# Kernel optimization log

Measured on AMD Instinct MI355X. Metric: run time of the kernel, lower is better.

The kernel has to match this reference:

```python
import jax, jax.numpy as jnp
import numpy as np
from jax import lax

DN = ('NCHW', 'OIHW', 'NCHW')
EPS = 1e-5  # PyTorch BatchNorm default eps


def _bn(x, g, b):
    # BatchNorm2d in training mode: batch statistics over (N, H, W), biased var
    m = jnp.mean(x, (0, 2, 3), keepdims=True)
    v = jnp.mean((x - m) ** 2, (0, 2, 3), keepdims=True)
    return (x - m) * lax.rsqrt(v + EPS) * g[None, :, None, None] + b[None, :, None, None]


def _conv(x, w, b):
    # Conv2d(k=4, stride=2, padding=1)
    y = lax.conv_general_dilated(x, w, (2, 2), ((1, 1), (1, 1)), dimension_numbers=DN)
    return y + b[None, :, None, None]


def _deconv(x, w, b):
    # ConvTranspose2d(k=4, stride=2, padding=1) == dilated-input conv, pad k-1-p=2
    y = lax.conv_general_dilated(x, w, (1, 1), ((2, 2), (2, 2)), lhs_dilation=(2, 2),
                                 dimension_numbers=DN)
    return y + b[None, :, None, None]


def reference(x, codebook, eW1, eb1, eg1, ebt1, eW2, eb2, eg2, ebt2, eW3, eb3, eg3, ebt3,
              dW1, db1, dg1, dbt1, dW2, db2, dg2, dbt2, dW3, db3, dg3, dbt3):
    # --- encoder ---
    h = jax.nn.relu(_bn(_conv(x, eW1, eb1), eg1, ebt1))
    h = jax.nn.relu(_bn(_conv(h, eW2, eb2), eg2, ebt2))
    z_e = jax.nn.relu(_bn(_conv(h, eW3, eb3), eg3, ebt3))  # [B, 64, H/8, W/8]
    # --- vector quantization ---
    zp = z_e.transpose(0, 2, 3, 1)                 # [B, h, w, D]
    D = zp.shape[-1]
    z = zp.reshape(-1, D)                          # [N, D]
    dist = (jnp.sum(z * z, axis=1, keepdims=True)
            + jnp.sum(codebook * codebook, axis=1)
            - 2.0 * (z @ codebook.T))              # [N, K] squared distances
    idx = jnp.argmin(dist, axis=1)                 # [N]
    quant = codebook[idx].reshape(zp.shape)        # gather == one-hot matmul
    e_loss = jnp.mean((lax.stop_gradient(quant) - zp) ** 2)
    q_loss = jnp.mean((quant - lax.stop_gradient(zp)) ** 2)
    loss = q_loss + e_loss
    # straight-through estimator
    q_st = (zp + lax.stop_gradient(quant - zp)).transpose(0, 3, 1, 2)  # [B, D, h, w]
    # --- decoder ---
    h = jax.nn.relu(_bn(_deconv(q_st, dW1, db1), dg1, dbt1))
    h = jax.nn.relu(_bn(_deconv(h, dW2, db2), dg2, dbt2))
    z_d = jnp.tanh(_bn(_deconv(h, dW3, db3), dg3, dbt3))
    return z_d, loss


def setup_inputs() -> dict:
    key = jax.random.key(0)
    ks = jax.random.split(key, 16)
    B, C, H, W = 64, 3, 256, 256
    K, D = 512, 64
    f32 = jnp.float32

    def w(k, shape, fan_in):
        return jax.random.normal(k, shape, f32) * np.float32(1.0 / np.sqrt(fan_in))

    inp = {}
    inp['x'] = jax.random.normal(ks[0], (B, C, H, W), f32)
    inp['codebook'] = jax.random.uniform(ks[1], (K, D), f32, -1.0 / K, 1.0 / K)
    # encoder: 3 -> 16 -> 32 -> 64, conv k=4
    inp['eW1'] = w(ks[2], (16, 3, 4, 4), 3 * 16);   inp['eb1'] = jnp.zeros(16, f32)
    inp['eg1'] = jnp.ones(16, f32);                 inp['ebt1'] = jnp.zeros(16, f32)
    inp['eW2'] = w(ks[3], (32, 16, 4, 4), 16 * 16); inp['eb2'] = jnp.zeros(32, f32)
    inp['eg2'] = jnp.ones(32, f32);                 inp['ebt2'] = jnp.zeros(32, f32)
    inp['eW3'] = w(ks[4], (64, 32, 4, 4), 32 * 16); inp['eb3'] = jnp.zeros(64, f32)
    inp['eg3'] = jnp.ones(64, f32);                 inp['ebt3'] = jnp.zeros(64, f32)
    # decoder: 64 -> 32 -> 16 -> 3, convtranspose k=4 (weights stored OIHW)
    inp['dW1'] = w(ks[5], (32, 64, 4, 4), 64 * 16); inp['db1'] = jnp.zeros(32, f32)
    inp['dg1'] = jnp.ones(32, f32);                 inp['dbt1'] = jnp.zeros(32, f32)
    inp['dW2'] = w(ks[6], (16, 32, 4, 4), 32 * 16); inp['db2'] = jnp.zeros(16, f32)
    inp['dg2'] = jnp.ones(16, f32);                 inp['dbt2'] = jnp.zeros(16, f32)
    inp['dW3'] = w(ks[7], (3, 16, 4, 4), 16 * 16);  inp['db3'] = jnp.zeros(3, f32)
    inp['dg3'] = jnp.ones(3, f32);                  inp['dbt3'] = jnp.zeros(3, f32)
    return inp
```

## Files before the change

### kernel.cpp

```cpp
#include <hip/hip_runtime.h>
#include <hip/hip_bf16.h>


#define EPS 1e-5

__global__ void zero_stats_k(double* s, int n) {
    int i = blockIdx.x * blockDim.x + threadIdx.x;
    if (i < n) s[i] = 0.0;
}

__global__ void convert_w_k(const float* __restrict__ w1, const float* __restrict__ w2,
                            const float* __restrict__ w3, double* __restrict__ w64) {
    int i = blockIdx.x * blockDim.x + threadIdx.x;
    if (i < 768) w64[i] = (double)w1[i];
    else if (i < 768 + 8192) w64[i] = (double)w2[i - 768];
    else if (i < 768 + 8192 + 32768) w64[i] = (double)w3[i - 768 - 8192];
}

__device__ __forceinline__ void block_reduce2(double v1, double v2,
                                              double* t1, double* t2) {
#pragma unroll
    for (int o = 32; o; o >>= 1) {
        v1 += __shfl_down(v1, o);
        v2 += __shfl_down(v2, o);
    }
    __shared__ double ls[4][2];
    int wid = threadIdx.x >> 6, lane = threadIdx.x & 63;
    if (lane == 0) { ls[wid][0] = v1; ls[wid][1] = v2; }
    __syncthreads();
    if (threadIdx.x == 0) {
        atomicAdd(t1, ls[0][0] + ls[1][0] + ls[2][0] + ls[3][0]);
        atomicAdd(t2, ls[0][1] + ls[1][1] + ls[2][1] + ls[3][1]);
    }
    __syncthreads();
}

__global__ void conv1_stats_k(const float* __restrict__ x, const double* __restrict__ w64,
                              const float* __restrict__ bias,
                              double* __restrict__ partials) {
    __shared__ float xs[3][6][258];
    __shared__ double lsw[4][32];
    int band = blockIdx.x, n = blockIdx.y, tid = threadIdx.x;
    double sums[16], sqs[16];
#pragma unroll
    for (int j = 0; j < 16; ++j) { sums[j] = 0.0; sqs[j] = 0.0; }
    for (int s8 = 0; s8 < 8; ++s8) {
        int strip = band * 8 + s8;
        int iyBase = 4 * strip - 1;
        __syncthreads();
        for (int idx = tid; idx < 3 * 6 * 258; idx += 256) {
            int ch = idx / 1548, rem = idx - ch * 1548, r = rem / 258, cc = rem - r * 258;
            int iy = iyBase + r, ix = cc - 1;
            float v = 0.f;
            if ((unsigned)iy < 256u && (unsigned)ix < 256u)
                v = x[(size_t)(n * 3 + ch) * 65536 + iy * 256 + ix];
            xs[ch][r][cc] = v;
        }
        __syncthreads();
        int lr = 2 * (tid >> 7), lc = 2 * (tid & 127);
        double xd[3][4][4];
#pragma unroll
        for (int ci = 0; ci < 3; ++ci)
#pragma unroll
            for (int ky = 0; ky < 4; ++ky)
#pragma unroll
                for (int kx = 0; kx < 4; ++kx)
                    xd[ci][ky][kx] = (double)xs[ci][lr + ky][lc + kx];
#pragma unroll
        for (int co = 0; co < 16; ++co) {
            double acc = (double)bias[co];
            const double* wp = w64 + co * 48;
#pragma unroll
            for (int ci = 0; ci < 3; ++ci)
#pragma unroll
                for (int ky = 0; ky < 4; ++ky)
#pragma unroll
                    for (int kx = 0; kx < 4; ++kx)
                        acc = fma(xd[ci][ky][kx], wp[ci * 16 + ky * 4 + kx], acc);
            sums[co] += acc;
            sqs[co] = fma(acc, acc, sqs[co]);
        }
    }
    double val[32];
#pragma unroll
    for (int j = 0; j < 16; ++j) { val[j] = sums[j]; val[16 + j] = sqs[j]; }
#pragma unroll
    for (int o = 32; o; o >>= 1)
#pragma unroll
        for (int j = 0; j < 32; ++j) val[j] += __shfl_down(val[j], o);
    int wid = tid >> 6, lane = tid & 63;
    if (lane == 0)
#pragma unroll
        for (int j = 0; j < 32; ++j) lsw[wid][j] = val[j];
    __syncthreads();
    if (tid < 32) {
        double p = lsw[0][tid] + lsw[1][tid] + lsw[2][tid] + lsw[3][tid];
        partials[(size_t)(n * 8 + band) * 32 + tid] = p;
    }
}

__global__ void reduce_stats_k(const double* __restrict__ partials,
                               double* __restrict__ stats) {
    int t = threadIdx.x;
    if (t < 32) {
        double s = 0.0;
        for (int i = 0; i < 512; ++i) s += partials[(size_t)i * 32 + t];
        stats[t] = s;
    }
}

__global__ void fused_conv2_k(const float* __restrict__ x, const double* __restrict__ w1_64,
                              const float* __restrict__ eb1, const float* __restrict__ eg1,
                              const float* __restrict__ ebt1, const double* __restrict__ w2_64,
                              const float* __restrict__ eb2, const double* __restrict__ stats,
                              float* __restrict__ h2) {
    __shared__ float xs[3][38][38];
    __shared__ float h1s[16][18][18];
    int tile = blockIdx.x, n = blockIdx.y, tid = threadIdx.x;
    int ty = tile >> 3, tx = tile & 7;
    int iyBase = 32 * ty - 3, ixBase = 32 * tx - 3;
    for (int idx = tid; idx < 3 * 38 * 38; idx += 256) {
        int ch = idx / 1444, rem = idx - ch * 1444, r = rem / 38, cc = rem - r * 38;
        int iy = iyBase + r, ix = ixBase + cc;
        float v = 0.f;
        if ((unsigned)iy < 256u && (unsigned)ix < 256u)
            v = x[(size_t)(n * 3 + ch) * 65536 + iy * 256 + ix];
        xs[ch][r][cc] = v;
    }
    __syncthreads();
    int hy0 = 16 * ty - 1, hx0 = 16 * tx - 1;
    for (int idx = tid; idx < 16 * 18 * 18; idx += 256) {
        int ci = idx / 324, rem = idx - ci * 324, r = rem / 18, cc = rem - r * 18;
        int hy = hy0 + r, hx = hx0 + cc;
        float val = 0.f;
        if ((unsigned)hy < 128u && (unsigned)hx < 128u) {
            double xd[3][4][4];
#pragma unroll
            for (int c3 = 0; c3 < 3; ++c3)
#pragma unroll
                for (int ky = 0; ky < 4; ++ky)
#pragma unroll
                    for (int kx = 0; kx < 4; ++kx)
                        xd[c3][ky][kx] = (double)xs[c3][2 * r + ky][2 * cc + kx];
            double acc = (double)eb1[ci];
            const double* wp = w1_64 + ci * 48;
#pragma unroll
            for (int c3 = 0; c3 < 3; ++c3)
#pragma unroll
                for (int ky = 0; ky < 4; ++ky)
#pragma unroll
                    for (int kx = 0; kx < 4; ++kx)
                        acc = fma(xd[c3][ky][kx], wp[c3 * 16 + ky * 4 + kx], acc);
            double m = stats[ci] * (1.0 / 1048576.0);
            double var = stats[16 + ci] * (1.0 / 1048576.0) - m * m;
            double sc = (double)eg1[ci] / sqrt(var + EPS);
            double sh = (double)ebt1[ci] - m * sc;
            double v = fma(acc, sc, sh);
            val = (float)(v > 0.0 ? v : 0.0);
        }
        h1s[ci][r][cc] = val;
    }
    __syncthreads();
    int s = tid & 63, ly = s >> 3, lx = s & 7;
    int cog = __builtin_amdgcn_readfirstlane((tid >> 6) * 8);
    double acc[8];
#pragma unroll
    for (int j = 0; j < 8; ++j) acc[j] = (double)eb2[cog + j];
    for (int ci = 0; ci < 16; ++ci) {
        double td[16];
#pragma unroll
        for (int ky = 0; ky < 4; ++ky)
#pragma unroll
            for (int kx = 0; kx < 4; ++kx)
                td[ky * 4 + kx] = (double)h1s[ci][2 * ly + ky][2 * lx + kx];
#pragma unroll
        for (int j = 0; j < 8; ++j) {
            const double* wp = w2_64 + ((cog + j) * 16 + ci) * 16;
#pragma unroll
            for (int k = 0; k < 16; ++k)
                acc[j] = fma(td[k], wp[k], acc[j]);
        }
    }
    int oy = 8 * ty + ly, ox = 8 * tx + lx;
#pragma unroll
    for (int j = 0; j < 8; ++j)
        h2[(size_t)(n * 32 + cog + j) * 4096 + oy * 64 + ox] = (float)acc[j];
}

__global__ void bn_stats_k(const float* __restrict__ y, double* __restrict__ sum,
                           double* __restrict__ sq, int C, int HW) {
    int c = blockIdx.x, n = blockIdx.y;
    const float* p = y + (size_t)(n * C + c) * HW;
    double s = 0.0, s2 = 0.0;
    for (int i = threadIdx.x; i < HW; i += blockDim.x) {
        double v = (double)p[i];
        s += v;
        s2 = fma(v, v, s2);
    }
    block_reduce2(s, s2, &sum[c], &sq[c]);
}

__device__ __forceinline__ void bn_consts(int tid, int C, const double* sum,
                                          const double* sq, const float* g,
                                          const float* b, double invCnt,
                                          double* scd, double* shd) {
    if (tid < C) {
        double m = sum[tid] * invCnt;
        double var = sq[tid] * invCnt - m * m;
        double sc = (double)g[tid] / sqrt(var + EPS);
        scd[tid] = sc;
        shd[tid] = (double)b[tid] - m * sc;
    }
}

__global__ void conv3_k(const float* __restrict__ h2, const double* __restrict__ w3_64,
                        const float* __restrict__ bias, const float* __restrict__ eg2,
                        const float* __restrict__ ebt2, const double* __restrict__ sum2,
                        const double* __restrict__ sq2, float* __restrict__ z3) {
    __shared__ float hs[32][6][66];
    __shared__ double scd[32], shd[32];
    int c = blockIdx.x, n = blockIdx.y, tid = threadIdx.x;
    bn_consts(tid, 32, sum2, sq2, eg2, ebt2, 1.0 / 262144.0, scd, shd);
    __syncthreads();
    int iyBase = 4 * c - 1;
    for (int idx = tid; idx < 32 * 6 * 66; idx += 256) {
        int ch = idx / 396, rem = idx - ch * 396, r = rem / 66, cc = rem - r * 66;
        int iy = iyBase + r, ix = cc - 1;
        float val = 0.f;
        if ((unsigned)iy < 64u && (unsigned)ix < 64u) {
            double v = fma((double)h2[(size_t)(n * 32 + ch) * 4096 + iy * 64 + ix],
                           scd[ch], shd[ch]);
            val = v > 0.0 ? (float)v : 0.f;
        }
        hs[ch][r][cc] = val;
    }
    __syncthreads();
    int s = tid & 63;
    int oy = 2 * c + (s >> 5), ox = s & 31;
    int lr = 2 * (s >> 5), lc = 2 * ox;
    int cog = __builtin_amdgcn_readfirstlane((tid >> 6) * 16);
    double acc[16];
#pragma unroll
    for (int j = 0; j < 16; ++j) acc[j] = (double)bias[cog + j];
    for (int ci = 0; ci < 32; ++ci) {
        double td[16];
#pragma unroll
        for (int ky = 0; ky < 4; ++ky)
#pragma unroll
            for (int kx = 0; kx < 4; ++kx)
                td[ky * 4 + kx] = (double)hs[ci][lr + ky][lc + kx];
#pragma unroll
        for (int j = 0; j < 16; ++j) {
            const double* wp = w3_64 + ((cog + j) * 32 + ci) * 16;
#pragma unroll
            for (int k = 0; k < 16; ++k)
                acc[j] = fma(td[k], wp[k], acc[j]);
        }
    }
#pragma unroll
    for (int j = 0; j < 16; ++j)
        z3[(size_t)(n * 64 + cog + j) * 1024 + oy * 32 + ox] = (float)acc[j];
}

__device__ __forceinline__ float np_sum64(const float* a) {
    float r[8];
#pragma unroll
    for (int j = 0; j < 8; ++j) r[j] = a[j];
#pragma unroll
    for (int m = 1; m < 8; ++m)
#pragma unroll
        for (int j = 0; j < 8; ++j) r[j] += a[m * 8 + j];
    return ((r[0] + r[1]) + (r[2] + r[3])) + ((r[4] + r[5]) + (r[6] + r[7]));
}

__global__ void scc_k(const float* __restrict__ cb, float* __restrict__ scc) {
    int k = blockIdx.x * blockDim.x + threadIdx.x;
    if (k >= 512) return;
    const float* c = cb + (k << 6);
    float cc[64];
#pragma unroll
    for (int d = 0; d < 64; ++d) cc[d] = c[d] * c[d];
    scc[k] = np_sum64(cc);
}

__global__ void vq_k(const float* __restrict__ zraw, const float* __restrict__ cb,
                     const float* __restrict__ scc, const float* __restrict__ eg3,
                     const float* __restrict__ ebt3, const double* __restrict__ sum3,
                     const double* __restrict__ sq3, float* __restrict__ quant,
                     double* __restrict__ lossAcc) {
    __shared__ double scd[64], shd[64];
    bn_consts(threadIdx.x, 64, sum3, sq3, eg3, ebt3, 1.0 / 65536.0, scd, shd);
    __syncthreads();
    int p = blockIdx.x * blockDim.x + threadIdx.x;
    int n = p >> 10, hw = p & 1023;
    const float* zp = zraw + (size_t)n * 65536 + hw;
    float z32[64], zz[64];
#pragma unroll
    for (int d = 0; d < 64; ++d) {
        double v = fma((double)zp[d * 1024], scd[d], shd[d]);
        z32[d] = v > 0.0 ? (float)v : 0.f;
        zz[d] = z32[d] * z32[d];
    }
    float sz = np_sum64(zz);
    float bestf = 3.4e38f;
    int bif = 0;
    for (int k = 0; k < 512; ++k) {
        const float* c = cb + (k << 6);
        float dot = 0.f;
#pragma unroll
        for (int d = 0; d < 64; ++d) dot = fmaf(z32[d], c[d], dot);
        float distf = (sz + scc[k]) - 2.f * dot;
        if (distf < bestf) { bestf = distf; bif = k; }
    }
    const float* c = cb + (bif << 6);
    float* qp = quant + (size_t)n * 65536 + hw;
    double dist = 0.0;
#pragma unroll
    for (int d = 0; d < 64; ++d) {
        double diff = (double)z32[d] - (double)c[d];
        dist = fma(diff, diff, dist);
        qp[d * 1024] = c[d];
    }
    double s = dist;
#pragma unroll
    for (int o = 32; o; o >>= 1) s += __shfl_down(s, o);
    if ((threadIdx.x & 63) == 0) atomicAdd(lossAcc, s);
}

__global__ void finalize_loss_k(const double* lossAcc, float* out, int idx) {
    if (threadIdx.x == 0 && blockIdx.x == 0)
        out[idx] = (float)(2.0 * (*lossAcc) / 4194304.0);
}

__global__ void deconv1_k(const float* __restrict__ in, const float* __restrict__ w,
                          const float* __restrict__ bias, float* __restrict__ out) {
    __shared__ float ls[64][4][34];
    int b = blockIdx.x, n = blockIdx.y, tid = threadIdx.x;
    int qy0 = 2 * b;
    for (int idx = tid; idx < 64 * 4 * 34; idx += 256) {
        int ch = idx / 136, rem = idx - ch * 136, r = rem / 34, cc = rem - r * 34;
        int iy = qy0 - 1 + r, ix = cc - 1;
        float v = 0.f;
        if ((unsigned)iy < 32u && (unsigned)ix < 32u)
            v = in[(size_t)(n * 64 + ch) * 1024 + iy * 32 + ix];
        ls[ch][r][cc] = v;
    }
    __syncthreads();
    int pt = tid & 63;
    int qy = qy0 + (pt >> 5), qx = pt & 31;
    int cog = (tid >> 6) * 8;
    int rb = qy - qy0;
    float acc[2][2][8];
#pragma unroll
    for (int dy = 0; dy < 2; ++dy)
#pragma unroll
        for (int dx = 0; dx < 2; ++dx)
#pragma unroll
            for (int j = 0; j < 8; ++j) acc[dy][dx][j] = bias[cog + j];
    for (int ci = 0; ci < 64; ++ci) {
        float v[3][3];
#pragma unroll
        for (int ry = 0; ry < 3; ++ry)
#pragma unroll
            for (int rx = 0; rx < 3; ++rx)
                v[ry][rx] = ls[ci][rb + ry][qx + rx];
#pragma unroll
        for (int j = 0; j < 8; ++j) {
            const float* wp = w + ((cog + j) * 64 + ci) * 16;
            acc[0][0][j] += v[0][0]*wp[0] + v[0][1]*wp[2] + v[1][0]*wp[8]  + v[1][1]*wp[10];
            acc[0][1][j] += v[0][1]*wp[1] + v[0][2]*wp[3] + v[1][1]*wp[9]  + v[1][2]*wp[11];
            acc[1][0][j] += v[1][0]*wp[4] + v[1][1]*wp[6] + v[2][0]*wp[12] + v[2][1]*wp[14];
            acc[1][1][j] += v[1][1]*wp[5] + v[1][2]*wp[7] + v[2][1]*wp[13] + v[2][2]*wp[15];
        }
    }
#pragma unroll
    for (int dy = 0; dy < 2; ++dy)
#pragma unroll
        for (int dx = 0; dx < 2; ++dx)
#pragma unroll
            for (int j = 0; j < 8; ++j)
                out[(size_t)(n * 32 + cog + j) * 4096 + (2*qy+dy) * 64 + 2*qx+dx]
                    = acc[dy][dx][j];
}

__global__ void deconv2_k(const float* __restrict__ in, const float* __restrict__ w,
                          const float* __restrict__ bias, const float* __restrict__ g,
                          const float* __restrict__ bt, const double* __restrict__ sum,
                          const double* __restrict__ sq, float* __restrict__ out) {
    __shared__ float ls[32][3][66];
    __shared__ double scd[32], shd[32];
    int b = blockIdx.x, n = blockIdx.y, tid = threadIdx.x;
    bn_consts(tid, 32, sum, sq, g, bt, 1.0 / 262144.0, scd, shd);
    __syncthreads();
    for (int idx = tid; idx < 32 * 3 * 66; idx += 256) {
        int ch = idx / 198, rem = idx - ch * 198, r = rem / 66, cc = rem - r * 66;
        int iy = b - 1 + r, ix = cc - 1;
        float val = 0.f;
        if ((unsigned)iy < 64u && (unsigned)ix < 64u) {
            double v = fma((double)in[(size_t)(n * 32 + ch) * 4096 + iy * 64 + ix],
                           scd[ch], shd[ch]);
            val = v > 0.0 ? (float)v : 0.f;
        }
        ls[ch][r][cc] = val;
    }
    __syncthreads();
    int qx = tid & 63;
    int cog = (tid >> 6) * 4;
    float acc[2][2][4];
#pragma unroll
    for (int dy = 0; dy < 2; ++dy)
#pragma unroll
        for (int dx = 0; dx < 2; ++dx)
#pragma unroll
            for (int j = 0; j < 4; ++j) acc[dy][dx][j] = bias[cog + j];
    for (int ci = 0; ci < 32; ++ci) {
        float v[3][3];
#pragma unroll
        for (int ry = 0; ry < 3; ++ry)
#pragma unroll
            for (int rx = 0; rx < 3; ++rx)
                v[ry][rx] = ls[ci][ry][qx + rx];
#pragma unroll
        for (int j = 0; j < 4; ++j) {
            const float* wp = w + ((cog + j) * 32 + ci) * 16;
            acc[0][0][j] += v[0][0]*wp[0] + v[0][1]*wp[2] + v[1][0]*wp[8]  + v[1][1]*wp[10];
            acc[0][1][j] += v[0][1]*wp[1] + v[0][2]*wp[3] + v[1][1]*wp[9]  + v[1][2]*wp[11];
            acc[1][0][j] += v[1][0]*wp[4] + v[1][1]*wp[6] + v[2][0]*wp[12] + v[2][1]*wp[14];
            acc[1][1][j] += v[1][1]*wp[5] + v[1][2]*wp[7] + v[2][1]*wp[13] + v[2][2]*wp[15];
        }
    }
#pragma unroll
    for (int dy = 0; dy < 2; ++dy)
#pragma unroll
        for (int dx = 0; dx < 2; ++dx)
#pragma unroll
            for (int j = 0; j < 4; ++j)
                out[(size_t)(n * 16 + cog + j) * 16384 + (2*b+dy) * 128 + 2*qx+dx]
                    = acc[dy][dx][j];
}

__global__ void deconv3_k(const float* __restrict__ in, const float* __restrict__ w,
                          const float* __restrict__ bias, const float* __restrict__ g,
                          const float* __restrict__ bt, const double* __restrict__ sum,
                          const double* __restrict__ sq, float* __restrict__ out) {
    __shared__ float ls[16][4][130];
    __shared__ double scd[16], shd[16];
    int b = blockIdx.x, n = blockIdx.y, tid = threadIdx.x;
    bn_consts(tid, 16, sum, sq, g, bt, 1.0 / 1048576.0, scd, shd);
    __syncthreads();
    int qy0 = 2 * b;
    for (int idx = tid; idx < 16 * 4 * 130; idx += 256) {
        int ch = idx / 520, rem = idx - ch * 520, r = rem / 130, cc = rem - r * 130;
        int iy = qy0 - 1 + r, ix = cc - 1;
        float val = 0.f;
        if ((unsigned)iy < 128u && (unsigned)ix < 128u) {
            double v = fma((double)in[(size_t)(n * 16 + ch) * 16384 + iy * 128 + ix],
                           scd[ch], shd[ch]);
            val = v > 0.0 ? (float)v : 0.f;
        }
        ls[ch][r][cc] = val;
    }
    __syncthreads();
    int qy = qy0 + (tid >> 7), qx = tid & 127;
    int rb = qy - qy0;
    float acc[2][2][3];
#pragma unroll
    for (int dy = 0; dy < 2; ++dy)
#pragma unroll
        for (int dx = 0; dx < 2; ++dx)
#pragma unroll
            for (int j = 0; j < 3; ++j) acc[dy][dx][j] = bias[j];
    for (int ci = 0; ci < 16; ++ci) {
        float v[3][3];
#pragma unroll
        for (int ry = 0; ry < 3; ++ry)
#pragma unroll
            for (int rx = 0; rx < 3; ++rx)
                v[ry][rx] = ls[ci][rb + ry][qx + rx];
#pragma unroll
        for (int j = 0; j < 3; ++j) {
            const float* wp = w + (j * 16 + ci) * 16;
            acc[0][0][j] += v[0][0]*wp[0] + v[0][1]*wp[2] + v[1][0]*wp[8]  + v[1][1]*wp[10];
            acc[0][1][j] += v[0][1]*wp[1] + v[0][2]*wp[3] + v[1][1]*wp[9]  + v[1][2]*wp[11];
            acc[1][0][j] += v[1][0]*wp[4] + v[1][1]*wp[6] + v[2][0]*wp[12] + v[2][1]*wp[14];
            acc[1][1][j] += v[1][1]*wp[5] + v[1][2]*wp[7] + v[2][1]*wp[13] + v[2][2]*wp[15];
        }
    }
#pragma unroll
    for (int dy = 0; dy < 2; ++dy)
#pragma unroll
        for (int dx = 0; dx < 2; ++dx)
#pragma unroll
            for (int j = 0; j < 3; ++j)
                out[(size_t)(n * 3 + j) * 65536 + (2*qy+dy) * 256 + 2*qx+dx]
                    = acc[dy][dx][j];
}

__global__ void bn_tanh_k(const float* __restrict__ y, const double* __restrict__ sum,
                          const double* __restrict__ sq, const float* __restrict__ g,
                          const float* __restrict__ b, float* __restrict__ out, int HW,
                          double invCnt) {
    int hw = blockIdx.x * blockDim.x + threadIdx.x;
    int c = blockIdx.y, n = blockIdx.z, C = gridDim.y;
    double m = sum[c] * invCnt;
    double var = sq[c] * invCnt - m * m;
    double sc = (double)g[c] / sqrt(var + EPS);
    double sh = (double)b[c] - m * sc;
    size_t i = (size_t)(n * C + c) * HW + hw;
    out[i] = (float)tanh(fma((double)y[i], sc, sh));
}

extern "C" void kernel_launch(void* const* d_in, const int* in_sizes, int n_in,
                              void* d_out, int out_size, void* d_ws, size_t ws_size,
                              hipStream_t stream) {
    const float* x   = (const float*)d_in[0];
    const float* cb  = (const float*)d_in[1];
    const float* eW1 = (const float*)d_in[2];
    const float* eb1 = (const float*)d_in[3];
    const float* eg1 = (const float*)d_in[4];
    const float* ebt1= (const float*)d_in[5];
    const float* eW2 = (const float*)d_in[6];
    const float* eb2 = (const float*)d_in[7];
    const float* eg2 = (const float*)d_in[8];
    const float* ebt2= (const float*)d_in[9];
    const float* eW3 = (const float*)d_in[10];
    const float* eb3 = (const float*)d_in[11];
    const float* eg3 = (const float*)d_in[12];
    const float* ebt3= (const float*)d_in[13];
    const float* dW1 = (const float*)d_in[14];
    const float* db1 = (const float*)d_in[15];
    const float* dg1 = (const float*)d_in[16];
    const float* dbt1= (const float*)d_in[17];
    const float* dW2 = (const float*)d_in[18];
    const float* db2 = (const float*)d_in[19];
    const float* dg2 = (const float*)d_in[20];
    const float* dbt2= (const float*)d_in[21];
    const float* dW3 = (const float*)d_in[22];
    const float* db3 = (const float*)d_in[23];
    const float* dg3 = (const float*)d_in[24];
    const float* dbt3= (const float*)d_in[25];

    float* out = (float*)d_out;
    char* ws = (char*)d_ws;
    float* h2    = (float*)ws;
    float* z     = (float*)(ws + 33554432);
    float* quant = (float*)(ws + 50331648);
    float* d1    = (float*)(ws + 67108864);
    float* d2    = (float*)ws;
    float* d3    = (float*)(ws + 67108864);
    double* partials = (double*)ws;
    double* w64  = (double*)(ws + 67108864);
    double* w1_64 = w64;
    double* w2_64 = w64 + 768;
    double* w3_64 = w64 + 768 + 8192;
    double* stats = (double*)(ws + 117440512);
    double* lossAcc = stats + 326;
    float* scc   = (float*)(ws + 117443200);
    dim3 B(256);

    zero_stats_k<<<2, B, 0, stream>>>(stats, 327);
    scc_k<<<2, B, 0, stream>>>(cb, scc);
    convert_w_k<<<163, B, 0, stream>>>(eW1, eW2, eW3, w64);

    conv1_stats_k<<<dim3(8, 64), B, 0, stream>>>(x, w1_64, eb1, partials);
    reduce_stats_k<<<1, 64, 0, stream>>>(partials, stats);
    fused_conv2_k<<<dim3(64, 64), B, 0, stream>>>(x, w1_64, eb1, eg1, ebt1, w2_64,
                                                  eb2, stats, h2);
    bn_stats_k<<<dim3(32, 64), B, 0, stream>>>(h2, stats + 32, stats + 64, 32, 4096);
    conv3_k<<<dim3(16, 64), B, 0, stream>>>(h2, w3_64, eb3, eg2, ebt2,
                                            stats + 32, stats + 64, z);
    bn_stats_k<<<dim3(64, 64), B, 0, stream>>>(z, stats + 96, stats + 160, 64, 1024);
    vq_k<<<256, B, 0, stream>>>(z, cb, scc, eg3, ebt3, stats + 96, stats + 160,
                                quant, lossAcc);
    finalize_loss_k<<<1, 64, 0, stream>>>(lossAcc, out, out_size - 1);

    deconv1_k<<<dim3(16, 64), B, 0, stream>>>(quant, dW1, db1, d1);
    bn_stats_k<<<dim3(32, 64), B, 0, stream>>>(d1, stats + 224, stats + 256, 32, 4096);
    deconv2_k<<<dim3(64, 64), B, 0, stream>>>(d1, dW2, db2, dg1, dbt1,
                                              stats + 224, stats + 256, d2);
    bn_stats_k<<<dim3(16, 64), B, 0, stream>>>(d2, stats + 288, stats + 304, 16, 16384);
    deconv3_k<<<dim3(64, 64), B, 0, stream>>>(d2, dW3, db3, dg2, dbt2,
                                              stats + 288, stats + 304, d3);
    bn_stats_k<<<dim3(3, 64), B, 0, stream>>>(d3, stats + 320, stats + 323, 3, 65536);
    bn_tanh_k<<<dim3(256, 3, 64), B, 0, stream>>>(d3, stats + 320, stats + 323,
                                                  dg3, dbt3, out, 65536,
                                                  1.0 / 4194304.0);
}
```

Measured before the change: 1.783 ms.

## Split conv1 stats and VQ search across more blocks, drop conv2 input staging

conv1_stats now launches four times as many blocks, each covering two strips instead of eight, and writes four times as many partials, which the reduction then sums. The VQ kernel splits the 512-entry codebook search into four 128-entry chunks per pixel across the block's waves and merges them through shared memory, giving four times as many blocks. fused_conv2 drops the shared-memory staging of the input tile and reads x directly from global memory inside the h1 computation. The aim is more parallelism on serial-heavy kernels, at the cost of a longer single-threaded partial reduction and redundant global loads in conv2.

```diff
diff --git a/kernel.cpp b/kernel.cpp
--- a/kernel.cpp
+++ b/kernel.cpp
@@ -44,8 +44,8 @@
     double sums[16], sqs[16];
 #pragma unroll
     for (int j = 0; j < 16; ++j) { sums[j] = 0.0; sqs[j] = 0.0; }
-    for (int s8 = 0; s8 < 8; ++s8) {
-        int strip = band * 8 + s8;
+    for (int s8 = 0; s8 < 2; ++s8) {
+        int strip = band * 2 + s8;
         int iyBase = 4 * strip - 1;
         __syncthreads();
         for (int idx = tid; idx < 3 * 6 * 258; idx += 256) {
@@ -95,7 +95,7 @@
     __syncthreads();
     if (tid < 32) {
         double p = lsw[0][tid] + lsw[1][tid] + lsw[2][tid] + lsw[3][tid];
-        partials[(size_t)(n * 8 + band) * 32 + tid] = p;
+        partials[(size_t)(n * 32 + band) * 32 + tid] = p;
     }
 }
 
@@ -104,7 +104,7 @@
     int t = threadIdx.x;
     if (t < 32) {
         double s = 0.0;
-        for (int i = 0; i < 512; ++i) s += partials[(size_t)i * 32 + t];
+        for (int i = 0; i < 2048; ++i) s += partials[(size_t)i * 32 + t];
         stats[t] = s;
     }
 }
@@ -114,34 +114,30 @@
                               const float* __restrict__ ebt1, const double* __restrict__ w2_64,
                               const float* __restrict__ eb2, const double* __restrict__ stats,
                               float* __restrict__ h2) {
-    __shared__ float xs[3][38][38];
     __shared__ float h1s[16][18][18];
     int tile = blockIdx.x, n = blockIdx.y, tid = threadIdx.x;
     int ty = tile >> 3, tx = tile & 7;
-    int iyBase = 32 * ty - 3, ixBase = 32 * tx - 3;
-    for (int idx = tid; idx < 3 * 38 * 38; idx += 256) {
-        int ch = idx / 1444, rem = idx - ch * 1444, r = rem / 38, cc = rem - r * 38;
-        int iy = iyBase + r, ix = ixBase + cc;
-        float v = 0.f;
-        if ((unsigned)iy < 256u && (unsigned)ix < 256u)
-            v = x[(size_t)(n * 3 + ch) * 65536 + iy * 256 + ix];
-        xs[ch][r][cc] = v;
-    }
-    __syncthreads();
     int hy0 = 16 * ty - 1, hx0 = 16 * tx - 1;
+    const float* xp = x + (size_t)n * 3 * 65536;
     for (int idx = tid; idx < 16 * 18 * 18; idx += 256) {
         int ci = idx / 324, rem = idx - ci * 324, r = rem / 18, cc = rem - r * 18;
         int hy = hy0 + r, hx = hx0 + cc;
         float val = 0.f;
         if ((unsigned)hy < 128u && (unsigned)hx < 128u) {
+            int iy0 = 2 * hy - 1, ix0 = 2 * hx - 1;
             double xd[3][4][4];
 #pragma unroll
             for (int c3 = 0; c3 < 3; ++c3)
 #pragma unroll
                 for (int ky = 0; ky < 4; ++ky)
 #pragma unroll
-                    for (int kx = 0; kx < 4; ++kx)
-                        xd[c3][ky][kx] = (double)xs[c3][2 * r + ky][2 * cc + kx];
+                    for (int kx = 0; kx < 4; ++kx) {
+                        int iy = iy0 + ky, ix = ix0 + kx;
+                        float v = 0.f;
+                        if ((unsigned)iy < 256u && (unsigned)ix < 256u)
+                            v = xp[(size_t)c3 * 65536 + iy * 256 + ix];
+                        xd[c3][ky][kx] = (double)v;
+                    }
             double acc = (double)eb1[ci];
             const double* wp = w1_64 + ci * 48;
 #pragma unroll
@@ -289,9 +285,12 @@
                      const double* __restrict__ sq3, float* __restrict__ quant,
                      double* __restrict__ lossAcc) {
     __shared__ double scd[64], shd[64];
+    __shared__ float bfs[256];
+    __shared__ int bis[256];
     bn_consts(threadIdx.x, 64, sum3, sq3, eg3, ebt3, 1.0 / 65536.0, scd, shd);
     __syncthreads();
-    int p = blockIdx.x * blockDim.x + threadIdx.x;
+    int chunk = threadIdx.x >> 6, pi = threadIdx.x & 63;
+    int p = blockIdx.x * 64 + pi;
     int n = p >> 10, hw = p & 1023;
     const float* zp = zraw + (size_t)n * 65536 + hw;
     float z32[64], zz[64];
@@ -302,9 +301,10 @@
         zz[d] = z32[d] * z32[d];
     }
     float sz = np_sum64(zz);
+    int k0 = chunk << 7;
     float bestf = 3.4e38f;
-    int bif = 0;
-    for (int k = 0; k < 512; ++k) {
+    int bif = k0;
+    for (int k = k0; k < k0 + 128; ++k) {
         const float* c = cb + (k << 6);
         float dot = 0.f;
 #pragma unroll
@@ -312,19 +312,29 @@
         float distf = (sz + scc[k]) - 2.f * dot;
         if (distf < bestf) { bestf = distf; bif = k; }
     }
-    const float* c = cb + (bif << 6);
-    float* qp = quant + (size_t)n * 65536 + hw;
-    double dist = 0.0;
-#pragma unroll
-    for (int d = 0; d < 64; ++d) {
-        double diff = (double)z32[d] - (double)c[d];
-        dist = fma(diff, diff, dist);
-        qp[d * 1024] = c[d];
-    }
-    double s = dist;
-#pragma unroll
-    for (int o = 32; o; o >>= 1) s += __shfl_down(s, o);
-    if ((threadIdx.x & 63) == 0) atomicAdd(lossAcc, s);
+    bfs[threadIdx.x] = bestf;
+    bis[threadIdx.x] = bif;
+    __syncthreads();
+    if (chunk == 0) {
+#pragma unroll
+        for (int c4 = 1; c4 < 4; ++c4) {
+            float v = bfs[c4 * 64 + pi];
+            if (v < bestf) { bestf = v; bif = bis[c4 * 64 + pi]; }
+        }
+        const float* c = cb + (bif << 6);
+        float* qp = quant + (size_t)n * 65536 + hw;
+        double dist = 0.0;
+#pragma unroll
+        for (int d = 0; d < 64; ++d) {
+            double diff = (double)z32[d] - (double)c[d];
+            dist = fma(diff, diff, dist);
+            qp[d * 1024] = c[d];
+        }
+        double s = dist;
+#pragma unroll
+        for (int o = 32; o; o >>= 1) s += __shfl_down(s, o);
+        if (pi == 0) atomicAdd(lossAcc, s);
+    }
 }
 
 __global__ void finalize_loss_k(const double* lossAcc, float* out, int idx) {
@@ -562,7 +572,7 @@
     scc_k<<<2, B, 0, stream>>>(cb, scc);
     convert_w_k<<<163, B, 0, stream>>>(eW1, eW2, eW3, w64);
 
-    conv1_stats_k<<<dim3(8, 64), B, 0, stream>>>(x, w1_64, eb1, partials);
+    conv1_stats_k<<<dim3(32, 64), B, 0, stream>>>(x, w1_64, eb1, partials);
     reduce_stats_k<<<1, 64, 0, stream>>>(partials, stats);
     fused_conv2_k<<<dim3(64, 64), B, 0, stream>>>(x, w1_64, eb1, eg1, ebt1, w2_64,
                                                   eb2, stats, h2);
@@ -570,8 +580,8 @@
     conv3_k<<<dim3(16, 64), B, 0, stream>>>(h2, w3_64, eb3, eg2, ebt2,
                                             stats + 32, stats + 64, z);
     bn_stats_k<<<dim3(64, 64), B, 0, stream>>>(z, stats + 96, stats + 160, 64, 1024);
-    vq_k<<<256, B, 0, stream>>>(z, cb, scc, eg3, ebt3, stats + 96, stats + 160,
-                                quant, lossAcc);
+    vq_k<<<1024, B, 0, stream>>>(z, cb, scc, eg3, ebt3, stats + 96, stats + 160,
+                                 quant, lossAcc);
     finalize_loss_k<<<1, 64, 0, stream>>>(lossAcc, out, out_size - 1);
 
     deconv1_k<<<dim3(16, 64), B, 0, stream>>>(quant, dW1, db1, d1);
```

Result: slower. 2.706 ms (+51.8%).
